# Performance work log

Hardware: AMD Instinct MI355X
Metric: run time of the kernel (lower is better)

Reference implementation:

```python
import jax, jax.numpy as jnp
import numpy as np

A_THRESH = 0.5  # module-level `a`
P_THRESH = 0.5  # module-level `p`
B, IN, H = 131072, 3, 256
D = IN + H


def setup_inputs() -> dict:
    key = jax.random.key(0)
    ks = jax.random.split(key, 7)
    lim = 1.0 / np.sqrt(D)  # torch nn.Linear default uniform(-1/sqrt(fan_in), ...)
    return {
        "input_tensor": jax.random.normal(ks[0], (B, IN), dtype=jnp.float32),
        "h_cur": jax.random.normal(ks[1], (B, H), dtype=jnp.float32),
        "c_cur": jax.random.normal(ks[2], (B, H), dtype=jnp.float32),
        # fused [i|f|g|o] gate weights, stored [in, out]
        "W_gates": jax.random.uniform(ks[3], (D, 4 * H), minval=-lim, maxval=lim, dtype=jnp.float32),
        "b_gates": jax.random.uniform(ks[4], (4 * H,), minval=-lim, maxval=lim, dtype=jnp.float32),
        # switch gates init.normal_(std=0.01), fused [w_i|w_g]
        "W_switch": 0.01 * jax.random.normal(ks[5], (D, 2), dtype=jnp.float32),
        "b_switch": 0.01 * jax.random.normal(ks[6], (2,), dtype=jnp.float32),
    }


def reference(input_tensor, h_cur, c_cur, W_gates, b_gates, W_switch, b_switch):
    combined = jnp.concatenate([input_tensor, h_cur], axis=1)  # [B, D]
    gates = combined @ W_gates + b_gates                       # [B, 4H]
    h = h_cur.shape[1]
    i = jax.nn.sigmoid(gates[:, :h])
    f = jax.nn.sigmoid(gates[:, h:2 * h])
    g = jnp.tanh(gates[:, 2 * h:3 * h])
    o = jax.nn.sigmoid(gates[:, 3 * h:])

    sw = jax.nn.sigmoid(combined @ W_switch + b_switch)        # [B, 2]
    w_i, w_g = sw[:, 0], sw[:, 1]

    n = w_g.shape[0]
    thr = n * A_THRESH
    cnt_g = jnp.sum(w_g > P_THRESH)
    cnt_i = jnp.sum(w_i > P_THRESH)

    fc = f * c_cur
    c_next_i = fc + i
    c_next_g = fc + g
    c_next_ig = fc + i * g

    cond_i = (cnt_g < thr) & (cnt_i > thr)
    cond_g = (cnt_g > thr) & (cnt_i < thr)
    c_next = jnp.where(cond_i, c_next_i, jnp.where(cond_g, c_next_g, c_next_ig))
    h_next = o * jnp.tanh(c_next)
    return h_next, c_next
```

## Files before the change

kernel.cpp:

```cpp
#include <hip/hip_runtime.h>

#define BROWS 131072

typedef __attribute__((ext_vector_type(8))) __bf16 bf16x8;
typedef __attribute__((ext_vector_type(4))) __bf16 bf16x4;
typedef __attribute__((ext_vector_type(4))) float f32x4;

__device__ __forceinline__ float sigmoidf_(float x) {
    return 1.0f / (1.0f + __expf(-x));
}
__device__ __forceinline__ float tanhf_(float x) {
    return 1.0f - 2.0f / (__expf(2.0f * x) + 1.0f);
}

__global__ void wt_kernel(const float* __restrict__ Wg, __bf16* __restrict__ WT) {
    int gid = blockIdx.x * 256 + threadIdx.x;
    int k = gid >> 10;
    int c = gid & 1023;
    float v = Wg[(3 + k) * 1024 + c];
    WT[c * 256 + k] = (__bf16)v;
}

__global__ void switch_kernel(const float* __restrict__ x, const float* __restrict__ h,
                              const float* __restrict__ Wsw, const float* __restrict__ bsw,
                              int* __restrict__ cnt) {
    const int lane = threadIdx.x & 63;
    const int gw = (blockIdx.x * blockDim.x + threadIdx.x) >> 6;
    const int nw = (gridDim.x * blockDim.x) >> 6;

    float w0[4], w1[4];
#pragma unroll
    for (int j = 0; j < 4; ++j) {
        int r = 3 + 4 * lane + j;
        w0[j] = Wsw[r * 2 + 0];
        w1[j] = Wsw[r * 2 + 1];
    }
    float wi0 = 0.0f, wi1 = 0.0f;
    if (lane < 3) { wi0 = Wsw[lane * 2 + 0]; wi1 = Wsw[lane * 2 + 1]; }
    const float b0 = bsw[0], b1 = bsw[1];

    int ci = 0, cg = 0;
    for (int row = gw; row < BROWS; row += nw) {
        const float4 hv = *(const float4*)(h + row * 256 + 4 * lane);
        float si = hv.x * w0[0] + hv.y * w0[1] + hv.z * w0[2] + hv.w * w0[3];
        float sg = hv.x * w1[0] + hv.y * w1[1] + hv.z * w1[2] + hv.w * w1[3];
        if (lane < 3) {
            float xv = x[row * 3 + lane];
            si += xv * wi0;
            sg += xv * wi1;
        }
#pragma unroll
        for (int off = 32; off >= 1; off >>= 1) {
            si += __shfl_xor(si, off, 64);
            sg += __shfl_xor(sg, off, 64);
        }
        if (lane == 0) {
            ci += (si + b0) > 0.0f;
            cg += (sg + b1) > 0.0f;
        }
    }
    if (lane == 0) {
        atomicAdd(&cnt[0], ci);
        atomicAdd(&cnt[1], cg);
    }
}

__global__ __launch_bounds__(256)
void lstm_main(const float* __restrict__ x,
               const float* __restrict__ h,
               const float* __restrict__ c_cur,
               const float* __restrict__ Wg,
               const float* __restrict__ bg,
               const __bf16* __restrict__ WT,
               const int* __restrict__ cnt,
               float* __restrict__ out) {
    __shared__ __bf16 A_lds[128 * 40];

    const int tid = threadIdx.x;
    const int lane = tid & 63;
    const int w = tid >> 6;
    const int q = lane >> 4;
    const int ln = lane & 15;
    const int m0 = blockIdx.y * 128;
    const int j0 = blockIdx.x * 32;
    const int wrow = (w >> 1) * 64;
    const int colh = j0 + (w & 1) * 16 + ln;

    const int ci = cnt[0], cg = cnt[1];
    const bool cond_i = (cg < 65536) && (ci > 65536);
    const bool cond_g = (cg > 65536) && (ci < 65536);

    f32x4 acc[4][4];
    float bcol[4], wx0[4], wx1[4], wx2[4];
#pragma unroll
    for (int nt = 0; nt < 4; ++nt) {
        int colg = nt * 256 + colh;
        bcol[nt] = bg[colg];
        wx0[nt] = Wg[0 * 1024 + colg];
        wx1[nt] = Wg[1 * 1024 + colg];
        wx2[nt] = Wg[2 * 1024 + colg];
    }
#pragma unroll
    for (int mt = 0; mt < 4; ++mt) {
#pragma unroll
        for (int r = 0; r < 4; ++r) {
            int row = m0 + wrow + mt * 16 + q * 4 + r;
            float x0 = x[row * 3 + 0];
            float x1 = x[row * 3 + 1];
            float x2 = x[row * 3 + 2];
#pragma unroll
            for (int nt = 0; nt < 4; ++nt) {
                acc[mt][nt][r] = bcol[nt] + x0 * wx0[nt] + x1 * wx1[nt] + x2 * wx2[nt];
            }
        }
    }

    float4 areg[4];
#pragma unroll
    for (int i = 0; i < 4; ++i) {
        int idx = tid + 256 * i;
        int row = idx >> 3, kq = idx & 7;
        areg[i] = *(const float4*)(h + (m0 + row) * 256 + 0 * 32 + kq * 4);
    }

    const __bf16* wtb[4];
#pragma unroll
    for (int nt = 0; nt < 4; ++nt)
        wtb[nt] = WT + (nt * 256 + colh) * 256 + q * 8;

    for (int kc = 0; kc < 8; ++kc) {
        if (kc) __syncthreads();
#pragma unroll
        for (int i = 0; i < 4; ++i) {
            int idx = tid + 256 * i;
            int row = idx >> 3, kq = idx & 7;
            bf16x4 v;
            v[0] = (__bf16)areg[i].x;
            v[1] = (__bf16)areg[i].y;
            v[2] = (__bf16)areg[i].z;
            v[3] = (__bf16)areg[i].w;
            *(bf16x4*)(&A_lds[row * 40 + kq * 4]) = v;
        }
        __syncthreads();
        if (kc < 7) {
#pragma unroll
            for (int i = 0; i < 4; ++i) {
                int idx = tid + 256 * i;
                int row = idx >> 3, kq = idx & 7;
                areg[i] = *(const float4*)(h + (m0 + row) * 256 + (kc + 1) * 32 + kq * 4);
            }
        }
        bf16x8 bfrag[4];
#pragma unroll
        for (int nt = 0; nt < 4; ++nt)
            bfrag[nt] = *(const bf16x8*)(wtb[nt] + kc * 32);
        bf16x8 afrag[4];
#pragma unroll
        for (int mt = 0; mt < 4; ++mt)
            afrag[mt] = *(const bf16x8*)(&A_lds[(wrow + mt * 16 + ln) * 40 + q * 8]);
#pragma unroll
        for (int mt = 0; mt < 4; ++mt)
#pragma unroll
            for (int nt = 0; nt < 4; ++nt)
                acc[mt][nt] = __builtin_amdgcn_mfma_f32_16x16x32_bf16(
                    afrag[mt], bfrag[nt], acc[mt][nt], 0, 0, 0);
    }

#pragma unroll
    for (int mt = 0; mt < 4; ++mt) {
#pragma unroll
        for (int r = 0; r < 4; ++r) {
            int row = m0 + wrow + mt * 16 + q * 4 + r;
            float gi = sigmoidf_(acc[mt][0][r]);
            float gf = sigmoidf_(acc[mt][1][r]);
            float gg = tanhf_(acc[mt][2][r]);
            float go = sigmoidf_(acc[mt][3][r]);
            float c = c_cur[row * 256 + colh];
            float X = cond_i ? gi : (cond_g ? gg : gi * gg);
            float cn = gf * c + X;
            float hn = go * tanhf_(cn);
            out[row * 256 + colh] = hn;
            out[BROWS * 256 + row * 256 + colh] = cn;
        }
    }
}

extern "C" void kernel_launch(void* const* d_in, const int* in_sizes, int n_in,
                              void* d_out, int out_size, void* d_ws, size_t ws_size,
                              hipStream_t stream) {
    const float* x   = (const float*)d_in[0];
    const float* h   = (const float*)d_in[1];
    const float* c   = (const float*)d_in[2];
    const float* Wg  = (const float*)d_in[3];
    const float* bg  = (const float*)d_in[4];
    const float* Wsw = (const float*)d_in[5];
    const float* bsw = (const float*)d_in[6];
    float* out = (float*)d_out;

    int* cnt = (int*)d_ws;
    __bf16* WT = (__bf16*)((char*)d_ws + 1024);

    hipMemsetAsync(d_ws, 0, 8, stream);
    wt_kernel<<<1024, 256, 0, stream>>>(Wg, WT);
    switch_kernel<<<1024, 256, 0, stream>>>(x, h, Wsw, bsw, cnt);
    lstm_main<<<dim3(8, 1024), 256, 0, stream>>>(x, h, c, Wg, bg, WT, cnt, out);
}
```

Before: 775.9 us.

## Restructure switch reduction per-row, vectorize weight transpose, remap LSTM block order

The switch kernel now assigns one row per thread. Rows of h are staged through padded shared memory and the per-warp counts are reduced with ballot/popcount, replacing the shuffle-reduction loop that handled one row per warp. The weight transpose kernel now writes 8 bf16 values per thread with a vector store. The main LSTM kernel uses a 1D grid with a swizzled block-to-tile mapping, so that the blocks sharing the same rows of h run close together in XCD/L2 scheduling. These changes target switch-kernel latency and cache reuse of h, at the cost of more shared-memory use in the switch kernel.

```diff
diff --git a/kernel.cpp b/kernel.cpp
--- a/kernel.cpp
+++ b/kernel.cpp
@@ -13,55 +13,65 @@
     return 1.0f - 2.0f / (__expf(2.0f * x) + 1.0f);
 }
 
-__global__ void wt_kernel(const float* __restrict__ Wg, __bf16* __restrict__ WT) {
+__global__ __launch_bounds__(256)
+void wt_kernel(const float* __restrict__ Wg, __bf16* __restrict__ WT) {
     int gid = blockIdx.x * 256 + threadIdx.x;
-    int k = gid >> 10;
-    int c = gid & 1023;
-    float v = Wg[(3 + k) * 1024 + c];
-    WT[c * 256 + k] = (__bf16)v;
-}
-
-__global__ void switch_kernel(const float* __restrict__ x, const float* __restrict__ h,
-                              const float* __restrict__ Wsw, const float* __restrict__ bsw,
-                              int* __restrict__ cnt) {
-    const int lane = threadIdx.x & 63;
-    const int gw = (blockIdx.x * blockDim.x + threadIdx.x) >> 6;
-    const int nw = (gridDim.x * blockDim.x) >> 6;
-
-    float w0[4], w1[4];
-#pragma unroll
-    for (int j = 0; j < 4; ++j) {
-        int r = 3 + 4 * lane + j;
-        w0[j] = Wsw[r * 2 + 0];
-        w1[j] = Wsw[r * 2 + 1];
-    }
-    float wi0 = 0.0f, wi1 = 0.0f;
-    if (lane < 3) { wi0 = Wsw[lane * 2 + 0]; wi1 = Wsw[lane * 2 + 1]; }
-    const float b0 = bsw[0], b1 = bsw[1];
-
-    int ci = 0, cg = 0;
-    for (int row = gw; row < BROWS; row += nw) {
-        const float4 hv = *(const float4*)(h + row * 256 + 4 * lane);
-        float si = hv.x * w0[0] + hv.y * w0[1] + hv.z * w0[2] + hv.w * w0[3];
-        float sg = hv.x * w1[0] + hv.y * w1[1] + hv.z * w1[2] + hv.w * w1[3];
-        if (lane < 3) {
-            float xv = x[row * 3 + lane];
-            si += xv * wi0;
-            sg += xv * wi1;
-        }
-#pragma unroll
-        for (int off = 32; off >= 1; off >>= 1) {
-            si += __shfl_xor(si, off, 64);
-            sg += __shfl_xor(sg, off, 64);
-        }
-        if (lane == 0) {
-            ci += (si + b0) > 0.0f;
-            cg += (sg + b1) > 0.0f;
-        }
-    }
-    if (lane == 0) {
-        atomicAdd(&cnt[0], ci);
-        atomicAdd(&cnt[1], cg);
+    int c = gid >> 5;
+    int k8 = (gid & 31) * 8;
+    bf16x8 v;
+#pragma unroll
+    for (int j = 0; j < 8; ++j)
+        v[j] = (__bf16)Wg[(3 + k8 + j) * 1024 + c];
+    *(bf16x8*)(WT + c * 256 + k8) = v;
+}
+
+__global__ __launch_bounds__(256)
+void switch_kernel(const float* __restrict__ x, const float* __restrict__ h,
+                   const float* __restrict__ Wsw, const float* __restrict__ bsw,
+                   int* __restrict__ cnt) {
+    __shared__ float hs[256 * 33];
+    __shared__ float wpk[512];
+    const int tid = threadIdx.x;
+    const int r0 = blockIdx.x * 256;
+
+    *(float2*)&wpk[2 * tid] = *(const float2*)&Wsw[(3 + tid) * 2];
+
+    const int row = r0 + tid;
+    const float x0 = x[row * 3 + 0];
+    const float x1 = x[row * 3 + 1];
+    const float x2 = x[row * 3 + 2];
+    float si = x0 * Wsw[0] + x1 * Wsw[2] + x2 * Wsw[4] + bsw[0];
+    float sg = x0 * Wsw[1] + x1 * Wsw[3] + x2 * Wsw[5] + bsw[1];
+
+    for (int kc = 0; kc < 8; ++kc) {
+        __syncthreads();
+#pragma unroll
+        for (int i = 0; i < 8; ++i) {
+            int idx = tid + 256 * i;
+            int r = idx >> 3;
+            int c4 = (idx & 7) * 4;
+            float4 v = *(const float4*)(h + (r0 + r) * 256 + kc * 32 + c4);
+            hs[r * 33 + c4 + 0] = v.x;
+            hs[r * 33 + c4 + 1] = v.y;
+            hs[r * 33 + c4 + 2] = v.z;
+            hs[r * 33 + c4 + 3] = v.w;
+        }
+        __syncthreads();
+#pragma unroll
+        for (int c2 = 0; c2 < 16; ++c2) {
+            float4 wv = *(const float4*)&wpk[kc * 64 + c2 * 4];
+            float v0 = hs[tid * 33 + c2 * 2 + 0];
+            float v1 = hs[tid * 33 + c2 * 2 + 1];
+            si += v0 * wv.x + v1 * wv.z;
+            sg += v0 * wv.y + v1 * wv.w;
+        }
+    }
+
+    unsigned long long bi = __ballot(si > 0.0f);
+    unsigned long long bgm = __ballot(sg > 0.0f);
+    if ((tid & 63) == 0) {
+        atomicAdd(&cnt[0], (int)__popcll(bi));
+        atomicAdd(&cnt[1], (int)__popcll(bgm));
     }
 }
 
@@ -81,8 +91,12 @@
     const int w = tid >> 6;
     const int q = lane >> 4;
     const int ln = lane & 15;
-    const int m0 = blockIdx.y * 128;
-    const int j0 = blockIdx.x * 32;
+
+    const int bid = blockIdx.x;
+    const int jseq = bid >> 3;
+    const int m0 = (((bid & 7) << 7) + (jseq >> 3)) << 7;
+    const int j0 = (jseq & 7) << 5;
+
     const int wrow = (w >> 1) * 64;
     const int colh = j0 + (w & 1) * 16 + ln;
 
@@ -201,7 +215,7 @@
     __bf16* WT = (__bf16*)((char*)d_ws + 1024);
 
     hipMemsetAsync(d_ws, 0, 8, stream);
-    wt_kernel<<<1024, 256, 0, stream>>>(Wg, WT);
-    switch_kernel<<<1024, 256, 0, stream>>>(x, h, Wsw, bsw, cnt);
-    lstm_main<<<dim3(8, 1024), 256, 0, stream>>>(x, h, c, Wg, bg, WT, cnt, out);
-}
+    wt_kernel<<<128, 256, 0, stream>>>(Wg, WT);
+    switch_kernel<<<512, 256, 0, stream>>>(x, h, Wsw, bsw, cnt);
+    lstm_main<<<8192, 256, 0, stream>>>(x, h, c, Wg, bg, WT, cnt, out);
+}
```

Measured after the change: 717.0 us. 7.6% less time.
